# Kernel optimization log

Hardware: AMD Instinct MI355X
Metric: run time of the kernel (lower is better)

## Reference

```python
import jax, jax.numpy as jnp
import numpy as np

PIXEL_SIZE = 0.1
PI = 3.141592653589793


def setup_inputs() -> dict:
    key = jax.random.key(0)
    batch = jax.random.normal(key, (128, 1, 512, 512), dtype=jnp.float32)
    return {"batch": batch}


def _hann_window(roi):
    # lin = linspace(-roi/2, roi/2, roi); r[i,j] = sqrt(lin[j]^2 + lin[i]^2)
    lin = jnp.linspace(-roi / 2, roi / 2, roi, dtype=jnp.float32)
    r = jnp.sqrt(lin[None, :] ** 2 + lin[:, None] ** 2)
    hann = 0.5 * (1.0 + jnp.cos(PI * r / (roi / 2)))
    hann = jnp.where(r > roi / 2, 0.0, hann)
    return hann  # [roi, roi]


def _radial_segments(roi, n_freq):
    # radialDst = round(sqrt(xx^2 + yy^2)) with x = arange(-cx, roi-cx)
    cx = roi // 2
    x = np.arange(-cx, roi - cx, dtype=np.float64)
    xx, yy = np.meshgrid(x, x, indexing="ij")
    rad = np.round(np.sqrt(xx ** 2 + yy ** 2)).astype(np.int32)
    # bins >= n_freq go into an overflow segment that is discarded
    seg = np.where(rad < n_freq, rad, n_freq)
    return jnp.asarray(seg.ravel())


def reference(batch):
    px = PIXEL_SIZE
    roi = batch.shape[-1]
    cx = roi // 2
    n_freq = cx + 1
    nyquist = 1.0 / (2.0 * px)

    # subtract per-ROI mean
    batch_nm = batch - jnp.mean(batch, axis=(2, 3), keepdims=True)

    # Hann-windowed 2D power spectrum, averaged over realizations
    hann = _hann_window(roi)[None, None, :, :]
    F = jnp.fft.fftshift(jnp.fft.fft2(batch_nm * hann, axes=(2, 3)), axes=(2, 3))
    ps = jnp.mean(jnp.abs(F) ** 2, axis=0)            # [1, roi, roi]
    nps2D = (px ** 2 / roi ** 2) * jnp.squeeze(ps)    # [roi, roi]

    # single-pass radial mean binning (replaces per-k boolean-mask loop)
    seg = _radial_segments(roi, n_freq)
    flat = nps2D.ravel()
    sums = jax.ops.segment_sum(flat, seg, num_segments=n_freq + 1)[:n_freq]
    counts = jax.ops.segment_sum(jnp.ones_like(flat), seg, num_segments=n_freq + 1)[:n_freq]
    nps1D = sums / counts

    f1D = jnp.linspace(0.0, nyquist, n_freq, dtype=jnp.float32)
    return nps1D, nps2D, f1D
```

## Files before the change

### kernel.cpp

```cpp
#include <hip/hip_runtime.h>
#include <hip/hip_fp16.h>

#define N 512
#define NF 257
#define NB 128
#define PI_F 3.14159265358979323846f
#define C_SQ2 0.70710678118654752440f

typedef float f2 __attribute__((ext_vector_type(2)));
__device__ __forceinline__ f2 F2(float x, float y) { f2 r; r.x = x; r.y = y; return r; }

__device__ __forceinline__ f2 cmul(f2 a, f2 b) {
    return a.xx * b + F2(-a.y, a.y) * b.yx;
}
__device__ __forceinline__ void bf(f2& a, f2& b) {
    f2 t = b;
    b = a - t;
    a = a + t;
}
__device__ __forceinline__ void bf_tw(f2& a, f2& b, f2 w) {
    f2 t = cmul(b, w);
    b = a - t;
    a = a + t;
}
__device__ __forceinline__ void bf_ni(f2& a, f2& b) {
    f2 t = F2(b.y, -b.x);
    b = a - t;
    a = a + t;
}
__device__ __forceinline__ void lds_order() {
    asm volatile("" ::: "memory");
}

__device__ __forceinline__ void fft_phaseA(f2 v[8]) {
    const f2 w64  = F2(C_SQ2, -C_SQ2);
    const f2 w192 = F2(-C_SQ2, -C_SQ2);
    bf(v[0], v[1]); bf(v[2], v[3]); bf(v[4], v[5]); bf(v[6], v[7]);
    bf(v[0], v[2]); bf_ni(v[1], v[3]); bf(v[4], v[6]); bf_ni(v[5], v[7]);
    bf(v[0], v[4]); bf_tw(v[1], v[5], w64); bf_ni(v[2], v[6]); bf_tw(v[3], v[7], w192);
}
__device__ __forceinline__ void fft_phaseBC(f2 v[8], f2 W1, f2 W1a,
                                            f2 W1n, f2 W1c, f2 W2,
                                            f2 W2n, f2 W3) {
    bf_tw(v[0], v[1], W3); bf_tw(v[2], v[3], W3); bf_tw(v[4], v[5], W3); bf_tw(v[6], v[7], W3);
    bf_tw(v[0], v[2], W2); bf_tw(v[1], v[3], W2n); bf_tw(v[4], v[6], W2); bf_tw(v[5], v[7], W2n);
    bf_tw(v[0], v[4], W1); bf_tw(v[1], v[5], W1a); bf_tw(v[2], v[6], W1n); bf_tw(v[3], v[7], W1c);
}

__device__ __forceinline__ void fft512_core(f2 v[8], f2* st, int l) {
    const f2 w64  = F2(C_SQ2, -C_SQ2);
    const f2 w192 = F2(-C_SQ2, -C_SQ2);
    int g = l >> 3, r = l & 7;
    lds_order();
    fft_phaseA(v);
#pragma unroll
    for (int e = 0; e < 8; e++) st[9 * l + e] = v[e];
    lds_order();
#pragma unroll
    for (int t = 0; t < 8; t++) v[t] = st[72 * g + 9 * t + r];
    float sn, cs;
    __sincosf(-(PI_F / 32.0f) * (float)r, &sn, &cs);
    f2 W1 = F2(cs, sn);
    f2 W2 = cmul(W1, W1);
    f2 W3 = cmul(W2, W2);
    f2 W2n = F2(W2.y, -W2.x);
    f2 W1a = cmul(W1, w64);
    f2 W1n = F2(W1.y, -W1.x);
    f2 W1c = cmul(W1, w192);
    fft_phaseBC(v, W1, W1a, W1n, W1c, W2, W2n, W3);
    lds_order();
#pragma unroll
    for (int t = 0; t < 8; t++) st[72 * g + 9 * t + r] = v[t];
    lds_order();
#pragma unroll
    for (int t = 0; t < 8; t++) v[t] = st[72 * t + l + (l >> 3)];
    __sincosf(-(PI_F / 256.0f) * (float)l, &sn, &cs);
    f2 Wc = F2(cs, sn);
    f2 w2 = cmul(Wc, Wc);
    f2 w4 = cmul(w2, w2);
    f2 w2n = F2(w2.y, -w2.x);
    f2 Wca = cmul(Wc, w64);
    f2 Wcn = F2(Wc.y, -Wc.x);
    f2 Wcc = cmul(Wc, w192);
    fft_phaseBC(v, Wc, Wca, Wcn, Wcc, w2, w2n, w4);
}

__device__ __forceinline__ void fft512_x2(f2 va[8], f2 vb[8], f2* st, int l) {
    const f2 w64  = F2(C_SQ2, -C_SQ2);
    const f2 w192 = F2(-C_SQ2, -C_SQ2);
    int g = l >> 3, r = l & 7;
    fft_phaseA(va); fft_phaseA(vb);
    lds_order();
#pragma unroll
    for (int e = 0; e < 8; e++) st[9 * l + e] = va[e];
    lds_order();
#pragma unroll
    for (int t = 0; t < 8; t++) va[t] = st[72 * g + 9 * t + r];
    lds_order();
#pragma unroll
    for (int e = 0; e < 8; e++) st[9 * l + e] = vb[e];
    lds_order();
#pragma unroll
    for (int t = 0; t < 8; t++) vb[t] = st[72 * g + 9 * t + r];
    float sn, cs;
    __sincosf(-(PI_F / 32.0f) * (float)r, &sn, &cs);
    f2 W1 = F2(cs, sn);
    f2 W2 = cmul(W1, W1);
    f2 W3 = cmul(W2, W2);
    f2 W2n = F2(W2.y, -W2.x);
    f2 W1a = cmul(W1, w64);
    f2 W1n = F2(W1.y, -W1.x);
    f2 W1c = cmul(W1, w192);
    fft_phaseBC(va, W1, W1a, W1n, W1c, W2, W2n, W3);
    fft_phaseBC(vb, W1, W1a, W1n, W1c, W2, W2n, W3);
    lds_order();
#pragma unroll
    for (int t = 0; t < 8; t++) st[72 * g + 9 * t + r] = va[t];
    lds_order();
#pragma unroll
    for (int t = 0; t < 8; t++) va[t] = st[72 * t + l + (l >> 3)];
    lds_order();
#pragma unroll
    for (int t = 0; t < 8; t++) st[72 * g + 9 * t + r] = vb[t];
    lds_order();
#pragma unroll
    for (int t = 0; t < 8; t++) vb[t] = st[72 * t + l + (l >> 3)];
    __sincosf(-(PI_F / 256.0f) * (float)l, &sn, &cs);
    f2 Wc = F2(cs, sn);
    f2 w2 = cmul(Wc, Wc);
    f2 w4 = cmul(w2, w2);
    f2 w2n = F2(w2.y, -w2.x);
    f2 Wca = cmul(Wc, w64);
    f2 Wcn = F2(Wc.y, -Wc.x);
    f2 Wcc = cmul(Wc, w192);
    fft_phaseBC(va, Wc, Wca, Wcn, Wcc, w2, w2n, w4);
    fft_phaseBC(vb, Wc, Wca, Wcn, Wcc, w2, w2n, w4);
}

__device__ __forceinline__ void unpack_rows(const f2 v[8], __half2* tile,
                                            int lr0, int lr1, int lh, int slp) {
#pragma unroll
    for (int t = 0; t <= 4; t++) {
        f2 a = v[7 - t];
        float zfx = __shfl(a.x, slp);
        float zfy = __shfl(a.y, slp);
        if (lh == 0) { f2 o = v[(8 - t) & 7]; zfx = o.x; zfy = o.y; }
        f2 z = v[t];
        int col = 64 * t + lh;
        if (col < NF) {
            tile[lr0 * 265 + col] = __floats2half2_rn(0.5f * (z.x + zfx), 0.5f * (z.y - zfy));
            tile[lr1 * 265 + col] = __floats2half2_rn(0.5f * (z.y + zfy), 0.5f * (zfx - z.x));
        }
    }
}

__global__ __launch_bounds__(256) void hanntab_zero_kernel(float* __restrict__ htab,
                                                           float* __restrict__ accH,
                                                           float* __restrict__ bins,
                                                           float* __restrict__ meanacc) {
    int i = blockIdx.x * 256 + threadIdx.x;
    int r = i >> 9, c = i & (N - 1);
    const float step = (float)N / (float)(N - 1);
    float a = -0.5f * (float)N + (float)r * step;
    float b = -0.5f * (float)N + (float)c * step;
    float rr = sqrtf(a * a + b * b);
    float h = (rr > 256.0f) ? 0.0f : 0.5f * (1.0f + cosf(rr * (PI_F / 256.0f)));
    htab[i] = h;
    if (i < NF * N) accH[i] = 0.0f;
    if (i < 2 * (NF + 1)) bins[i] = 0.0f;
    if (i < NB) meanacc[i] = 0.0f;
}

__global__ __launch_bounds__(512) void hannfft_kernel(const float* __restrict__ htab,
                                                      f2* __restrict__ Hrow) {
    __shared__ __align__(16) float sm[9216];
    int tid = threadIdx.x;
    int w = tid >> 6, l = tid & 63;
    int rowbase = blockIdx.x << 4;
    int r1 = rowbase + 2 * w;
    int lh = __brev((unsigned)l) >> 26;
    int slp = __brev((unsigned)((64 - lh) & 63)) >> 26;
    const int bre[8] = {0, 4, 2, 6, 1, 5, 3, 7};
    const float* h1 = htab + (size_t)r1 * N + l;
    const float* h2 = h1 + N;

    f2 v[8];
#pragma unroll
    for (int e = 0; e < 8; e++) {
        int o = bre[e] << 6;
        v[e] = F2(h1[o], h2[o]);
    }

    f2* st = (f2*)sm + w * 576;
    fft512_core(v, st, lh);
    __syncthreads();

    float* tre = sm;
    float* tim = sm + 4240;
    int lr0 = 2 * w, lr1 = lr0 + 1;
#pragma unroll
    for (int t = 0; t <= 4; t++) {
        f2 a = v[7 - t];
        float zfx = __shfl(a.x, slp);
        float zfy = __shfl(a.y, slp);
        if (lh == 0) { f2 o = v[(8 - t) & 7]; zfx = o.x; zfy = o.y; }
        f2 z = v[t];
        int col = 64 * t + lh;
        if (col < NF) {
            tre[lr0 * 265 + col] = 0.5f * (z.x + zfx);
            tim[lr0 * 265 + col] = 0.5f * (z.y - zfy);
            tre[lr1 * 265 + col] = 0.5f * (z.y + zfy);
            tim[lr1 * 265 + col] = 0.5f * (zfx - z.x);
        }
    }
    __syncthreads();

    int c0 = tid >> 4, rr = tid & 15;
#pragma unroll
    for (int it = 0; it < 9; it++) {
        int c = it * 32 + c0;
        if (c < NF) {
            Hrow[(size_t)c * N + rowbase + rr] = F2(tre[rr * 265 + c], tim[rr * 265 + c]);
        }
    }
}

__global__ __launch_bounds__(512, 6) void rowfft_kernel(const float* __restrict__ x,
                                                        const float* __restrict__ htab,
                                                        float* __restrict__ meanacc,
                                                        __half2* __restrict__ inter) {
    __shared__ __align__(16) float sm[9216];
    __shared__ float redsum[8];
    int tid = threadIdx.x;
    int w = tid >> 6, l = tid & 63;
    int img = blockIdx.x >> 4;
    int rowbase = (blockIdx.x & 15) << 5;
    int r1 = rowbase + 4 * w;
    int lh = __brev((unsigned)l) >> 26;
    int slp = __brev((unsigned)((64 - lh) & 63)) >> 26;
    const int bre[8] = {0, 4, 2, 6, 1, 5, 3, 7};
    const float* xp = x + ((size_t)img * N + r1) * N + l;
    const float* hp = htab + (size_t)r1 * N + l;

    float ax[4][8], hx[4][8];
#pragma unroll
    for (int j = 0; j < 4; j++)
#pragma unroll
        for (int e = 0; e < 8; e++) ax[j][e] = xp[j * N + (bre[e] << 6)];
#pragma unroll
    for (int j = 0; j < 4; j++)
#pragma unroll
        for (int e = 0; e < 8; e++) hx[j][e] = hp[j * N + (bre[e] << 6)];
    __builtin_amdgcn_sched_barrier(0);

    float rsum = 0.0f;
#pragma unroll
    for (int j = 0; j < 4; j++)
#pragma unroll
        for (int e = 0; e < 8; e++) rsum += ax[j][e];

    f2 va[8], vb[8];
#pragma unroll
    for (int e = 0; e < 8; e++) {
        va[e] = F2(ax[0][e] * hx[0][e], ax[1][e] * hx[1][e]);
        vb[e] = F2(ax[2][e] * hx[2][e], ax[3][e] * hx[3][e]);
    }

#pragma unroll
    for (int off = 32; off > 0; off >>= 1) rsum += __shfl_down(rsum, off);
    if (l == 0) redsum[w] = rsum;

    f2* st = (f2*)sm + w * 576;
    fft512_x2(va, vb, st, lh);
    __syncthreads();
    if (tid == 0) {
        float s = 0.0f;
#pragma unroll
        for (int i = 0; i < 8; i++) s += redsum[i];
        atomicAdd(meanacc + img, s);
    }

    __half2* tile = (__half2*)sm;
    unpack_rows(va, tile, 4 * w, 4 * w + 1, lh, slp);
    unpack_rows(vb, tile, 4 * w + 2, 4 * w + 3, lh, slp);
    __syncthreads();

    int c0 = tid >> 5, rr = tid & 31;
#pragma unroll
    for (int it = 0; it < 17; it++) {
        int c = it * 16 + c0;
        if (c < NF) {
            inter[((size_t)img * NF + c) * N + rowbase + rr] = tile[rr * 265 + c];
        }
    }
}

__global__ __launch_bounds__(256, 4) void colfft_kernel(const __half2* __restrict__ inter,
                                                        const f2* __restrict__ Hrow,
                                                        const float* __restrict__ meanacc,
                                                        float* __restrict__ accH) {
    __shared__ __align__(16) float sm[4608];
    int tid = threadIdx.x;
    int w = tid >> 6, l = tid & 63;
    int col = blockIdx.x * 4 + w;
    int colc = col < NF ? col : NF - 1;
    int b0 = blockIdx.y * 4;
    f2* st = (f2*)sm + w * 576;
    int lh = __brev((unsigned)l) >> 26;
    const int bre[8] = {0, 4, 2, 6, 1, 5, 3, 7};

    f2 hc[8];
    const f2* hp = Hrow + (size_t)colc * N + l;
#pragma unroll
    for (int e = 0; e < 8; e++) hc[e] = hp[bre[e] << 6];

    float mn[4];
#pragma unroll
    for (int i = 0; i < 4; i++)
        mn[i] = meanacc[b0 + i] * (1.0f / ((float)N * (float)N));

    float pw[8];
#pragma unroll
    for (int t = 0; t < 8; t++) pw[t] = 0.0f;

    const size_t istr = (size_t)NF * N;
    const __half2* base = inter + ((size_t)b0 * NF + colc) * N + l;

    __half2 cA[8], cB[8], nA[8], nB[8];
#pragma unroll
    for (int e = 0; e < 8; e++) {
        cA[e] = base[bre[e] << 6];
        cB[e] = base[istr + (bre[e] << 6)];
    }
    __builtin_amdgcn_sched_barrier(0);

#pragma unroll
    for (int it = 0; it < 2; it++) {
        if (it == 0) {
#pragma unroll
            for (int e = 0; e < 8; e++) {
                nA[e] = base[2 * istr + (bre[e] << 6)];
                nB[e] = base[3 * istr + (bre[e] << 6)];
            }
        }
        float mA = mn[2 * it], mB = mn[2 * it + 1];
        f2 va[8], vb[8];
#pragma unroll
        for (int e = 0; e < 8; e++) {
            float2 zA = __half22float2(cA[e]);
            float2 zB = __half22float2(cB[e]);
            va[e] = F2(zA.x, zA.y) - mA * hc[e];
            vb[e] = F2(zB.x, zB.y) - mB * hc[e];
        }
        fft512_x2(va, vb, st, lh);
#pragma unroll
        for (int t = 0; t < 8; t++)
            pw[t] += va[t].x * va[t].x + va[t].y * va[t].y
                   + vb[t].x * vb[t].x + vb[t].y * vb[t].y;
#pragma unroll
        for (int e = 0; e < 8; e++) { cA[e] = nA[e]; cB[e] = nB[e]; }
    }

    if (col < NF) {
#pragma unroll
        for (int t = 0; t < 8; t++)
            atomicAdd(&accH[(size_t)col * N + 64 * t + lh], pw[t]);
    }
}

__global__ __launch_bounds__(256) void finalize2d_kernel(const float* __restrict__ accH,
                                                         float* __restrict__ out2d,
                                                         float* __restrict__ bins) {
    __shared__ float lsum[NF];
    __shared__ float lcnt[NF];
    int t = threadIdx.x;
    for (int i = t; i < NF; i += 256) { lsum[i] = 0.0f; lcnt[i] = 0.0f; }
    __syncthreads();
    const float scale = (0.1f * 0.1f) / ((float)N * (float)N) / (float)NB;
    int idx = blockIdx.x * 256 + t;
    int stride = gridDim.x * 256;
    for (int p = idx; p < N * N; p += stride) {
        int i = p >> 9, j = p & (N - 1);
        int jm = (j + 256) & 511;
        int col, k;
        if (jm < NF) { col = jm; k = (i + 256) & 511; }
        else         { col = 256 - j; k = (256 - i) & 511; }
        float v = accH[((size_t)col << 9) + k] * scale;
        out2d[p] = v;
        float xi = (float)(i - 256), yj = (float)(j - 256);
        int rad = (int)rintf(sqrtf(xi * xi + yj * yj));
        if (rad < NF) { atomicAdd(&lsum[rad], v); atomicAdd(&lcnt[rad], 1.0f); }
    }
    __syncthreads();
    for (int i = t; i < NF; i += 256) {
        if (lsum[i] != 0.0f || lcnt[i] != 0.0f) {
            atomicAdd(&bins[i], lsum[i]);
            atomicAdd(&bins[NF + 1 + i], lcnt[i]);
        }
    }
}

__global__ void finalize1d_kernel(const float* __restrict__ bins, float* __restrict__ out) {
    int t = blockIdx.x * blockDim.x + threadIdx.x;
    if (t < NF) {
        out[t] = bins[t] / bins[NF + 1 + t];
        out[NF + N * N + t] = (float)t * (5.0f / 256.0f);
    }
}

extern "C" void kernel_launch(void* const* d_in, const int* in_sizes, int n_in,
                              void* d_out, int out_size, void* d_ws, size_t ws_size,
                              hipStream_t stream) {
    const float* x = (const float*)d_in[0];
    float* out = (float*)d_out;
    char* ws = (char*)d_ws;

    float* accH    = (float*)ws;
    float* meanacc = (float*)(ws + (size_t)NF * N * sizeof(float));
    float* bins    = meanacc + NB;
    size_t off_h = (size_t)NF * N * sizeof(float) + NB * sizeof(float)
                   + 2 * (NF + 1) * sizeof(float);
    off_h = (off_h + 255) & ~(size_t)255;
    f2* Hrow = (f2*)(ws + off_h);
    size_t off_t = off_h + (size_t)NF * N * sizeof(f2);
    off_t = (off_t + 255) & ~(size_t)255;
    float* htab = (float*)(ws + off_t);
    size_t off_inter = off_t + (size_t)N * N * sizeof(float);
    off_inter = (off_inter + 255) & ~(size_t)255;
    __half2* inter = (__half2*)(ws + off_inter);

    hanntab_zero_kernel<<<dim3(N * N / 256), dim3(256), 0, stream>>>(htab, accH, bins, meanacc);
    hannfft_kernel<<<dim3(32), dim3(512), 0, stream>>>(htab, Hrow);
    rowfft_kernel<<<dim3(NB * 16), dim3(512), 0, stream>>>(x, htab, meanacc, inter);
    colfft_kernel<<<dim3(65, 32), dim3(256), 0, stream>>>(inter, Hrow, meanacc, accH);
    finalize2d_kernel<<<dim3(512), dim3(256), 0, stream>>>(accH, out + NF, bins);
    finalize1d_kernel<<<dim3(2), dim3(256), 0, stream>>>(bins, out);
}
```

Before: 262.0 us.

## Merge Hann FFT into row FFT, process image pairs, fold 1D finalize

Removes two kernel launches. The Hann-window FFT moves into extra blocks of the row FFT kernel, and the 1D radial division is done by whichever finalize2d block finishes last, detected with an atomic counter. Each row-FFT block now handles two images, reusing the loaded Hann rows and halving the block count. In exchange, register pressure rises (launch bounds drop from 6 to 4 blocks), and a last-block-done pattern with threadfence is added, which relies on correct memory ordering.

```diff
diff --git a/kernel.cpp b/kernel.cpp
--- a/kernel.cpp
+++ b/kernel.cpp
@@ -6,6 +6,7 @@
 #define NB 128
 #define PI_F 3.14159265358979323846f
 #define C_SQ2 0.70710678118654752440f
+#define CNT (2 * (NF + 1))
 
 typedef float f2 __attribute__((ext_vector_type(2)));
 __device__ __forceinline__ f2 F2(float x, float y) { f2 r; r.x = x; r.y = y; return r; }
@@ -45,44 +46,6 @@
     bf_tw(v[0], v[1], W3); bf_tw(v[2], v[3], W3); bf_tw(v[4], v[5], W3); bf_tw(v[6], v[7], W3);
     bf_tw(v[0], v[2], W2); bf_tw(v[1], v[3], W2n); bf_tw(v[4], v[6], W2); bf_tw(v[5], v[7], W2n);
     bf_tw(v[0], v[4], W1); bf_tw(v[1], v[5], W1a); bf_tw(v[2], v[6], W1n); bf_tw(v[3], v[7], W1c);
-}
-
-__device__ __forceinline__ void fft512_core(f2 v[8], f2* st, int l) {
-    const f2 w64  = F2(C_SQ2, -C_SQ2);
-    const f2 w192 = F2(-C_SQ2, -C_SQ2);
-    int g = l >> 3, r = l & 7;
-    lds_order();
-    fft_phaseA(v);
-#pragma unroll
-    for (int e = 0; e < 8; e++) st[9 * l + e] = v[e];
-    lds_order();
-#pragma unroll
-    for (int t = 0; t < 8; t++) v[t] = st[72 * g + 9 * t + r];
-    float sn, cs;
-    __sincosf(-(PI_F / 32.0f) * (float)r, &sn, &cs);
-    f2 W1 = F2(cs, sn);
-    f2 W2 = cmul(W1, W1);
-    f2 W3 = cmul(W2, W2);
-    f2 W2n = F2(W2.y, -W2.x);
-    f2 W1a = cmul(W1, w64);
-    f2 W1n = F2(W1.y, -W1.x);
-    f2 W1c = cmul(W1, w192);
-    fft_phaseBC(v, W1, W1a, W1n, W1c, W2, W2n, W3);
-    lds_order();
-#pragma unroll
-    for (int t = 0; t < 8; t++) st[72 * g + 9 * t + r] = v[t];
-    lds_order();
-#pragma unroll
-    for (int t = 0; t < 8; t++) v[t] = st[72 * t + l + (l >> 3)];
-    __sincosf(-(PI_F / 256.0f) * (float)l, &sn, &cs);
-    f2 Wc = F2(cs, sn);
-    f2 w2 = cmul(Wc, Wc);
-    f2 w4 = cmul(w2, w2);
-    f2 w2n = F2(w2.y, -w2.x);
-    f2 Wca = cmul(Wc, w64);
-    f2 Wcn = F2(Wc.y, -Wc.x);
-    f2 Wcc = cmul(Wc, w192);
-    fft_phaseBC(v, Wc, Wca, Wcn, Wcc, w2, w2n, w4);
 }
 
 __device__ __forceinline__ void fft512_x2(f2 va[8], f2 vb[8], f2* st, int l) {
@@ -150,6 +113,23 @@
         if (col < NF) {
             tile[lr0 * 265 + col] = __floats2half2_rn(0.5f * (z.x + zfx), 0.5f * (z.y - zfy));
             tile[lr1 * 265 + col] = __floats2half2_rn(0.5f * (z.y + zfy), 0.5f * (zfx - z.x));
+        }
+    }
+}
+
+__device__ __forceinline__ void unpack_rows_store(const f2 v[8], f2* __restrict__ Hrow,
+                                                  int r0, int r1, int lh, int slp) {
+#pragma unroll
+    for (int t = 0; t <= 4; t++) {
+        f2 a = v[7 - t];
+        float zfx = __shfl(a.x, slp);
+        float zfy = __shfl(a.y, slp);
+        if (lh == 0) { f2 o = v[(8 - t) & 7]; zfx = o.x; zfy = o.y; }
+        f2 z = v[t];
+        int col = 64 * t + lh;
+        if (col < NF) {
+            Hrow[(size_t)col * N + r0] = F2(0.5f * (z.x + zfx), 0.5f * (z.y - zfy));
+            Hrow[(size_t)col * N + r1] = F2(0.5f * (z.y + zfy), 0.5f * (zfx - z.x));
         }
     }
 }
@@ -167,130 +147,126 @@
     float h = (rr > 256.0f) ? 0.0f : 0.5f * (1.0f + cosf(rr * (PI_F / 256.0f)));
     htab[i] = h;
     if (i < NF * N) accH[i] = 0.0f;
-    if (i < 2 * (NF + 1)) bins[i] = 0.0f;
+    if (i < CNT + 1) bins[i] = 0.0f;
     if (i < NB) meanacc[i] = 0.0f;
 }
 
-__global__ __launch_bounds__(512) void hannfft_kernel(const float* __restrict__ htab,
-                                                      f2* __restrict__ Hrow) {
+__global__ __launch_bounds__(512, 4) void rowfft_kernel(const float* __restrict__ x,
+                                                        const float* __restrict__ htab,
+                                                        float* __restrict__ meanacc,
+                                                        __half2* __restrict__ inter,
+                                                        f2* __restrict__ Hrow) {
     __shared__ __align__(16) float sm[9216];
+    __shared__ float redsum[16];
     int tid = threadIdx.x;
     int w = tid >> 6, l = tid & 63;
-    int rowbase = blockIdx.x << 4;
-    int r1 = rowbase + 2 * w;
     int lh = __brev((unsigned)l) >> 26;
     int slp = __brev((unsigned)((64 - lh) & 63)) >> 26;
     const int bre[8] = {0, 4, 2, 6, 1, 5, 3, 7};
-    const float* h1 = htab + (size_t)r1 * N + l;
-    const float* h2 = h1 + N;
-
-    f2 v[8];
-#pragma unroll
-    for (int e = 0; e < 8; e++) {
-        int o = bre[e] << 6;
-        v[e] = F2(h1[o], h2[o]);
-    }
-
     f2* st = (f2*)sm + w * 576;
-    fft512_core(v, st, lh);
-    __syncthreads();
-
-    float* tre = sm;
-    float* tim = sm + 4240;
-    int lr0 = 2 * w, lr1 = lr0 + 1;
-#pragma unroll
-    for (int t = 0; t <= 4; t++) {
-        f2 a = v[7 - t];
-        float zfx = __shfl(a.x, slp);
-        float zfy = __shfl(a.y, slp);
-        if (lh == 0) { f2 o = v[(8 - t) & 7]; zfx = o.x; zfy = o.y; }
-        f2 z = v[t];
-        int col = 64 * t + lh;
-        if (col < NF) {
-            tre[lr0 * 265 + col] = 0.5f * (z.x + zfx);
-            tim[lr0 * 265 + col] = 0.5f * (z.y - zfy);
-            tre[lr1 * 265 + col] = 0.5f * (z.y + zfy);
-            tim[lr1 * 265 + col] = 0.5f * (zfx - z.x);
-        }
-    }
-    __syncthreads();
-
-    int c0 = tid >> 4, rr = tid & 15;
-#pragma unroll
-    for (int it = 0; it < 9; it++) {
-        int c = it * 32 + c0;
-        if (c < NF) {
-            Hrow[(size_t)c * N + rowbase + rr] = F2(tre[rr * 265 + c], tim[rr * 265 + c]);
-        }
-    }
-}
-
-__global__ __launch_bounds__(512, 6) void rowfft_kernel(const float* __restrict__ x,
-                                                        const float* __restrict__ htab,
-                                                        float* __restrict__ meanacc,
-                                                        __half2* __restrict__ inter) {
-    __shared__ __align__(16) float sm[9216];
-    __shared__ float redsum[8];
-    int tid = threadIdx.x;
-    int w = tid >> 6, l = tid & 63;
-    int img = blockIdx.x >> 4;
+
+    if (blockIdx.x >= (NB / 2) * 16) {
+        int hb = blockIdx.x - (NB / 2) * 16;
+        int r1 = (hb << 5) + 4 * w;
+        const float* hp = htab + (size_t)r1 * N + l;
+        float hx[4][8];
+#pragma unroll
+        for (int j = 0; j < 4; j++)
+#pragma unroll
+            for (int e = 0; e < 8; e++) hx[j][e] = hp[j * N + (bre[e] << 6)];
+        f2 va[8], vb[8];
+#pragma unroll
+        for (int e = 0; e < 8; e++) {
+            va[e] = F2(hx[0][e], hx[1][e]);
+            vb[e] = F2(hx[2][e], hx[3][e]);
+        }
+        fft512_x2(va, vb, st, lh);
+        unpack_rows_store(va, Hrow, r1, r1 + 1, lh, slp);
+        unpack_rows_store(vb, Hrow, r1 + 2, r1 + 3, lh, slp);
+        return;
+    }
+
+    int ipair = blockIdx.x >> 4;
+    int img0 = 2 * ipair, img1 = img0 + 1;
     int rowbase = (blockIdx.x & 15) << 5;
     int r1 = rowbase + 4 * w;
-    int lh = __brev((unsigned)l) >> 26;
-    int slp = __brev((unsigned)((64 - lh) & 63)) >> 26;
-    const int bre[8] = {0, 4, 2, 6, 1, 5, 3, 7};
-    const float* xp = x + ((size_t)img * N + r1) * N + l;
-    const float* hp = htab + (size_t)r1 * N + l;
-
-    float ax[4][8], hx[4][8];
+    const float* xp0 = x + ((size_t)img0 * N + r1) * N + l;
+    const float* xp1 = x + ((size_t)img1 * N + r1) * N + l;
+    const float* hp  = htab + (size_t)r1 * N + l;
+
+    float ax[4][8], bx[4][8], hx[4][8];
 #pragma unroll
     for (int j = 0; j < 4; j++)
 #pragma unroll
-        for (int e = 0; e < 8; e++) ax[j][e] = xp[j * N + (bre[e] << 6)];
+        for (int e = 0; e < 8; e++) ax[j][e] = xp0[j * N + (bre[e] << 6)];
+#pragma unroll
+    for (int j = 0; j < 4; j++)
+#pragma unroll
+        for (int e = 0; e < 8; e++) bx[j][e] = xp1[j * N + (bre[e] << 6)];
 #pragma unroll
     for (int j = 0; j < 4; j++)
 #pragma unroll
         for (int e = 0; e < 8; e++) hx[j][e] = hp[j * N + (bre[e] << 6)];
     __builtin_amdgcn_sched_barrier(0);
 
-    float rsum = 0.0f;
+    float rs0 = 0.0f, rs1 = 0.0f;
 #pragma unroll
     for (int j = 0; j < 4; j++)
 #pragma unroll
-        for (int e = 0; e < 8; e++) rsum += ax[j][e];
-
-    f2 va[8], vb[8];
+        for (int e = 0; e < 8; e++) { rs0 += ax[j][e]; rs1 += bx[j][e]; }
+
+    f2 va[8], vb[8], vc[8], vd[8];
 #pragma unroll
     for (int e = 0; e < 8; e++) {
         va[e] = F2(ax[0][e] * hx[0][e], ax[1][e] * hx[1][e]);
         vb[e] = F2(ax[2][e] * hx[2][e], ax[3][e] * hx[3][e]);
-    }
-
-#pragma unroll
-    for (int off = 32; off > 0; off >>= 1) rsum += __shfl_down(rsum, off);
-    if (l == 0) redsum[w] = rsum;
-
-    f2* st = (f2*)sm + w * 576;
+        vc[e] = F2(bx[0][e] * hx[0][e], bx[1][e] * hx[1][e]);
+        vd[e] = F2(bx[2][e] * hx[2][e], bx[3][e] * hx[3][e]);
+    }
+
+#pragma unroll
+    for (int off = 32; off > 0; off >>= 1) {
+        rs0 += __shfl_down(rs0, off);
+        rs1 += __shfl_down(rs1, off);
+    }
+    if (l == 0) { redsum[w] = rs0; redsum[8 + w] = rs1; }
+
     fft512_x2(va, vb, st, lh);
     __syncthreads();
     if (tid == 0) {
-        float s = 0.0f;
-#pragma unroll
-        for (int i = 0; i < 8; i++) s += redsum[i];
-        atomicAdd(meanacc + img, s);
-    }
-
+        float s0 = 0.0f, s1 = 0.0f;
+#pragma unroll
+        for (int i = 0; i < 8; i++) { s0 += redsum[i]; s1 += redsum[8 + i]; }
+        atomicAdd(meanacc + img0, s0);
+        atomicAdd(meanacc + img1, s1);
+    }
     __half2* tile = (__half2*)sm;
     unpack_rows(va, tile, 4 * w, 4 * w + 1, lh, slp);
     unpack_rows(vb, tile, 4 * w + 2, 4 * w + 3, lh, slp);
     __syncthreads();
-
-    int c0 = tid >> 5, rr = tid & 31;
-#pragma unroll
-    for (int it = 0; it < 17; it++) {
-        int c = it * 16 + c0;
-        if (c < NF) {
-            inter[((size_t)img * NF + c) * N + rowbase + rr] = tile[rr * 265 + c];
+    {
+        int c0 = tid >> 5, rr = tid & 31;
+#pragma unroll
+        for (int it = 0; it < 17; it++) {
+            int c = it * 16 + c0;
+            if (c < NF)
+                inter[((size_t)img0 * NF + c) * N + rowbase + rr] = tile[rr * 265 + c];
+        }
+    }
+    __syncthreads();
+
+    fft512_x2(vc, vd, st, lh);
+    __syncthreads();
+    unpack_rows(vc, tile, 4 * w, 4 * w + 1, lh, slp);
+    unpack_rows(vd, tile, 4 * w + 2, 4 * w + 3, lh, slp);
+    __syncthreads();
+    {
+        int c0 = tid >> 5, rr = tid & 31;
+#pragma unroll
+        for (int it = 0; it < 17; it++) {
+            int c = it * 16 + c0;
+            if (c < NF)
+                inter[((size_t)img1 * NF + c) * N + rowbase + rr] = tile[rr * 265 + c];
         }
     }
 }
@@ -369,10 +345,12 @@
 }
 
 __global__ __launch_bounds__(256) void finalize2d_kernel(const float* __restrict__ accH,
-                                                         float* __restrict__ out2d,
+                                                         float* __restrict__ out,
                                                          float* __restrict__ bins) {
     __shared__ float lsum[NF];
     __shared__ float lcnt[NF];
+    __shared__ int lastflag;
+    float* out2d = out + NF;
     int t = threadIdx.x;
     for (int i = t; i < NF; i += 256) { lsum[i] = 0.0f; lcnt[i] = 0.0f; }
     __syncthreads();
@@ -398,13 +376,20 @@
             atomicAdd(&bins[NF + 1 + i], lcnt[i]);
         }
     }
-}
-
-__global__ void finalize1d_kernel(const float* __restrict__ bins, float* __restrict__ out) {
-    int t = blockIdx.x * blockDim.x + threadIdx.x;
-    if (t < NF) {
-        out[t] = bins[t] / bins[NF + 1 + t];
-        out[NF + N * N + t] = (float)t * (5.0f / 256.0f);
+    __threadfence();
+    __syncthreads();
+    if (t == 0) {
+        float old = atomicAdd(&bins[CNT], 1.0f);
+        lastflag = (old == (float)(gridDim.x - 1)) ? 1 : 0;
+    }
+    __syncthreads();
+    if (lastflag) {
+        for (int i = t; i < NF; i += 256) {
+            float s = atomicAdd(&bins[i], 0.0f);
+            float c = atomicAdd(&bins[NF + 1 + i], 0.0f);
+            out[i] = s / c;
+            out[NF + N * N + i] = (float)i * (5.0f / 256.0f);
+        }
     }
 }
 
@@ -419,7 +404,7 @@
     float* meanacc = (float*)(ws + (size_t)NF * N * sizeof(float));
     float* bins    = meanacc + NB;
     size_t off_h = (size_t)NF * N * sizeof(float) + NB * sizeof(float)
-                   + 2 * (NF + 1) * sizeof(float);
+                   + (CNT + 1) * sizeof(float);
     off_h = (off_h + 255) & ~(size_t)255;
     f2* Hrow = (f2*)(ws + off_h);
     size_t off_t = off_h + (size_t)NF * N * sizeof(f2);
@@ -430,9 +415,7 @@
     __half2* inter = (__half2*)(ws + off_inter);
 
     hanntab_zero_kernel<<<dim3(N * N / 256), dim3(256), 0, stream>>>(htab, accH, bins, meanacc);
-    hannfft_kernel<<<dim3(32), dim3(512), 0, stream>>>(htab, Hrow);
-    rowfft_kernel<<<dim3(NB * 16), dim3(512), 0, stream>>>(x, htab, meanacc, inter);
+    rowfft_kernel<<<dim3((NB / 2) * 16 + 16), dim3(512), 0, stream>>>(x, htab, meanacc, inter, Hrow);
     colfft_kernel<<<dim3(65, 32), dim3(256), 0, stream>>>(inter, Hrow, meanacc, accH);
-    finalize2d_kernel<<<dim3(512), dim3(256), 0, stream>>>(accH, out + NF, bins);
-    finalize1d_kernel<<<dim3(2), dim3(256), 0, stream>>>(bins, out);
-}
+    finalize2d_kernel<<<dim3(512), dim3(256), 0, stream>>>(accH, out, bins);
+}
```

Result: slower. 308.4 us (+17.7%).
